# Performance work log

Hardware: AMD Instinct MI355X
Metric: run time of the kernel (lower is better)

## Reference

```python
import jax, jax.numpy as jnp
import numpy as np

B, T, D, H = 2, 2048, 1024, 16
HS = D // H  # head_size = 64


def setup_inputs() -> dict:
    key = jax.random.key(0)
    ks = jax.random.split(key, 8)
    scale = D ** -0.5
    q = jax.random.normal(ks[0], (B, T, D), dtype=jnp.float32)
    k = jax.random.normal(ks[1], (B, T, D), dtype=jnp.float32)
    v = jax.random.normal(ks[2], (B, T, D), dtype=jnp.float32)
    # per-head projection weights (no bias), stacked over heads: [H, D, HS]
    Wq = jax.random.normal(ks[3], (H, D, HS), dtype=jnp.float32) * scale
    Wk = jax.random.normal(ks[4], (H, D, HS), dtype=jnp.float32) * scale
    Wv = jax.random.normal(ks[5], (H, D, HS), dtype=jnp.float32) * scale
    # output projection Linear(H*HS, D) with bias
    Wo = jax.random.normal(ks[6], (D, D), dtype=jnp.float32) * scale
    bo = jnp.zeros((D,), dtype=jnp.float32)
    # causal mask, broadcastable to [B, T, T]; mask==0 -> -inf
    mask = jnp.tril(jnp.ones((T, T), dtype=bool))[None]
    return {"q": q, "k": k, "v": v, "Wq": Wq, "Wk": Wk, "Wv": Wv,
            "Wo": Wo, "bo": bo, "mask": mask}


def reference(q, k, v, Wq, Wk, Wv, Wo, bo, mask):
    # Batched equivalent of the per-head loop: project all heads at once.
    Q = jnp.einsum('btc,hcd->bhtd', q, Wq)  # [B,H,T,HS]
    K = jnp.einsum('btc,hcd->bhtd', k, Wk)
    V = jnp.einsum('btc,hcd->bhtd', v, Wv)
    wei = jnp.einsum('bhtd,bhsd->bhts', Q, K) * (HS ** -0.5)  # [B,H,T,T]
    wei = jnp.where(mask[:, None, :, :], wei, jnp.float32(-jnp.inf))
    attn = jax.nn.softmax(wei, axis=-1)  # dropout is identity in eval
    out = jnp.einsum('bhts,bhsd->bhtd', attn, V)
    out = out.transpose(0, 2, 1, 3).reshape(B, T, D)  # concat heads
    return out @ Wo + bo
```

## Files before the change

kernel.cpp:

```cpp
#include <hip/hip_runtime.h>
#include <hip/hip_bf16.h>
#include <math.h>

#define BB 2
#define TT 2048
#define DM 1024
#define NH 16
#define HS 64
#define MM (BB*TT)

typedef __attribute__((ext_vector_type(8))) short s16x8;
typedef __attribute__((ext_vector_type(4))) float f32x4;

#define MFMA16(a,b,c) __builtin_amdgcn_mfma_f32_16x16x32_bf16((a),(b),(c),0,0,0)

__device__ inline unsigned short f2bf(float f) {
    union { float f; unsigned u; } x; x.f = f;
    unsigned r = x.u + 0x7fff + ((x.u >> 16) & 1);
    return (unsigned short)(r >> 16);
}
__device__ inline unsigned short f2bfr(float f) {
    union { float f; unsigned u; } x; x.f = f;
    return (unsigned short)((x.u + 0x8000u) >> 16);
}

__device__ __forceinline__ void gload16(const void* g, void* l) {
    __builtin_amdgcn_global_load_lds(
        (const __attribute__((address_space(1))) unsigned int*)g,
        (__attribute__((address_space(3))) unsigned int*)l, 16, 0, 0);
}

__global__ __launch_bounds__(256) void cvt_w_kernel(
    const float* __restrict__ W0, const float* __restrict__ W1,
    const float* __restrict__ W2, unsigned short* __restrict__ dst, int wo_mode)
{
    __shared__ __align__(16) short Tt[64 * 72];
    const int t = threadIdx.x;
    const int d0 = blockIdx.x * 64;
    const int h  = blockIdx.y;
    const int z  = blockIdx.z;
    const float* W = (z == 0) ? W0 : (z == 1) ? W1 : W2;
    unsigned short* dz = dst + (size_t)z * DM * DM;

    const int hs4 = (t & 15) * 4;
    const int dl0 = t >> 4;
    #pragma unroll
    for (int it = 0; it < 4; ++it) {
        int dl = it * 16 + dl0;
        const float* src = wo_mode
            ? &W[(size_t)(d0 + dl) * DM + h * 64 + hs4]
            : &W[(size_t)h * DM * HS + (size_t)(d0 + dl) * HS + hs4];
        float4 vv = *(const float4*)src;
        Tt[(hs4 + 0) * 72 + dl] = (short)f2bf(vv.x);
        Tt[(hs4 + 1) * 72 + dl] = (short)f2bf(vv.y);
        Tt[(hs4 + 2) * 72 + dl] = (short)f2bf(vv.z);
        Tt[(hs4 + 3) * 72 + dl] = (short)f2bf(vv.w);
    }
    __syncthreads();
    int hs = t >> 2, doff = (t & 3) * 16;
    s16x8 r0 = *(s16x8*)&Tt[hs * 72 + doff];
    s16x8 r1 = *(s16x8*)&Tt[hs * 72 + doff + 8];
    unsigned short* op = dz + (size_t)(h * 64 + hs) * DM + d0 + doff;
    *(s16x8*)op = r0;
    *(s16x8*)(op + 8) = r1;
}

__global__ __launch_bounds__(512) void proj_gemm_kernel(
    const float* __restrict__ q, const float* __restrict__ k,
    const float* __restrict__ v, const unsigned short* __restrict__ Wt,
    unsigned short* __restrict__ Qb, unsigned short* __restrict__ Kb,
    unsigned short* __restrict__ Vt)
{
    __shared__ __align__(16) unsigned short As[2][128 * 32];
    __shared__ __align__(16) unsigned short Bs[2][128 * 32];

    const int tid = threadIdx.x;
    const int l = tid & 63, w = tid >> 6;
    const int wr = w >> 2, wc = w & 3;
    const int g = l >> 4, r16 = l & 15;

    const int bid = blockIdx.x;
    const int xcd = bid & 7, u = bid >> 3;
    const int z = u >> 5, vv = u & 31;
    const int n0 = (vv >> 2) * 128;
    const int m0 = (xcd * 4 + (vv & 3)) * 128;

    const float* x = (z == 0) ? q : (z == 1) ? k : v;
    const unsigned short* Wz = Wt + (size_t)z * DM * DM;

    const int ar = tid >> 2, aq = tid & 3;
    const float* axp = x + (size_t)(m0 + ar) * DM + aq * 8;
    const int axr = (ar >> 1) & 3;
    const int awof = ar * 32 + ((aq ^ axr) * 8);

    const int brow = tid >> 2, bgl = tid & 3;
    const unsigned short* bS = Wz + (size_t)(n0 + brow) * DM
                             + ((bgl ^ ((brow >> 1) & 3)) * 8);
    const int bDof = tid * 8;

    int aoff[4], boff[2];
    #pragma unroll
    for (int i = 0; i < 4; ++i) {
        int row = wr * 64 + i * 16 + r16;
        aoff[i] = row * 32 + ((g ^ ((row >> 1) & 3)) * 8);
    }
    #pragma unroll
    for (int c = 0; c < 2; ++c) {
        int row = wc * 32 + c * 16 + r16;
        boff[c] = row * 32 + ((g ^ ((row >> 1) & 3)) * 8);
    }

    f32x4 acc[4][2];
    #pragma unroll
    for (int i = 0; i < 4; ++i)
        #pragma unroll
        for (int c = 0; c < 2; ++c)
            #pragma unroll
            for (int j = 0; j < 4; ++j) acc[i][c][j] = 0.0f;

    float4 al0, al1;

    #define PLOADA(k0_) do {                                             \
        const float* ap = axp + (k0_);                                   \
        al0 = *(const float4*)(ap);                                      \
        al1 = *(const float4*)(ap + 4);                                  \
    } while (0)

    #define GLOADB(buf, k0_) gload16(bS + (k0_), &Bs[(buf)][bDof])

    #define PSTORE(buf) do {                                             \
        union { s16x8 v; __hip_bfloat162 h[4]; } c0;                     \
        c0.h[0] = __float22bfloat162_rn(make_float2(al0.x, al0.y));      \
        c0.h[1] = __float22bfloat162_rn(make_float2(al0.z, al0.w));      \
        c0.h[2] = __float22bfloat162_rn(make_float2(al1.x, al1.y));      \
        c0.h[3] = __float22bfloat162_rn(make_float2(al1.z, al1.w));      \
        *(s16x8*)&As[(buf)][awof] = c0.v;                                \
    } while (0)

    #define PCOMPUTE(buf) do {                                           \
        s16x8 af[4], bf[2];                                              \
        _Pragma("unroll")                                                \
        for (int i = 0; i < 4; ++i) af[i] = *(const s16x8*)&As[(buf)][aoff[i]]; \
        _Pragma("unroll")                                                \
        for (int c = 0; c < 2; ++c) bf[c] = *(const s16x8*)&Bs[(buf)][boff[c]]; \
        _Pragma("unroll")                                                \
        for (int i = 0; i < 4; ++i)                                      \
            _Pragma("unroll")                                            \
            for (int c = 0; c < 2; ++c)                                  \
                acc[i][c] = MFMA16(af[i], bf[c], acc[i][c]);             \
    } while (0)

    PLOADA(0);
    GLOADB(0, 0);
    PSTORE(0);
    for (int t = 0; t < 31; ++t) {
        const int cur = t & 1;
        PLOADA((t + 1) * 32);
        GLOADB(cur ^ 1, (t + 1) * 32);
        asm volatile("s_waitcnt vmcnt(3) lgkmcnt(0)" ::: "memory");
        __builtin_amdgcn_sched_barrier(0);
        __builtin_amdgcn_s_barrier();
        PCOMPUTE(cur);
        PSTORE(cur ^ 1);
        __builtin_amdgcn_s_barrier();
    }
    asm volatile("s_waitcnt vmcnt(0) lgkmcnt(0)" ::: "memory");
    __builtin_amdgcn_sched_barrier(0);
    __builtin_amdgcn_s_barrier();
    PCOMPUTE(1);
    #undef PLOADA
    #undef GLOADB
    #undef PSTORE
    #undef PCOMPUTE

    const int h = (n0 >> 6) + (wc >> 1);
    const int hsb = (wc & 1) * 32;
    if (z != 2) {
        unsigned short* dst = (z == 0) ? Qb : Kb;
        const float sc = (z == 0) ? 0.18033688011112042f : 1.0f;
        #pragma unroll
        for (int i = 0; i < 4; ++i)
            #pragma unroll
            for (int j = 0; j < 4; ++j) {
                int row = m0 + wr * 64 + i * 16 + g * 4 + j;
                int bb = row >> 11, tt = row & (TT - 1);
                size_t rb = (((size_t)(bb * NH + h)) * TT + tt) * HS;
                #pragma unroll
                for (int c = 0; c < 2; ++c)
                    dst[rb + hsb + c * 16 + r16] = f2bf(acc[i][c][j] * sc);
            }
    } else {
        #pragma unroll
        for (int i = 0; i < 4; ++i) {
            int row0 = m0 + wr * 64 + i * 16 + g * 4;
            int bb = row0 >> 11, tt0 = row0 & (TT - 1);
            #pragma unroll
            for (int c = 0; c < 2; ++c) {
                int hs = hsb + c * 16 + r16;
                union { unsigned long long u; unsigned short s[4]; } pk;
                #pragma unroll
                for (int j = 0; j < 4; ++j) pk.s[j] = f2bf(acc[i][c][j]);
                *(unsigned long long*)&Vt[(((size_t)(bb * NH + h)) * HS + hs) * TT + tt0] = pk.u;
            }
        }
    }
}

__global__ __launch_bounds__(512) void out_gemm_kernel(
    const unsigned short* __restrict__ Ob, const unsigned short* __restrict__ Wot,
    const float* __restrict__ bo, float* __restrict__ out)
{
    __shared__ __align__(16) unsigned short As2[2][128 * 32];
    __shared__ __align__(16) unsigned short Bs2[2][128 * 32];

    const int tid = threadIdx.x;
    const int l = tid & 63, w = tid >> 6;
    const int wr = w >> 2, wc = w & 3;
    const int g = l >> 4, r16 = l & 15;

    const int bid = blockIdx.x;
    const int xcd = bid & 7, u = bid >> 3;
    const int n0 = (u >> 2) * 128;
    const int m0 = (xcd * 4 + (u & 3)) * 128;

    const int srow = tid >> 2, sgl = tid & 3;
    const int scol = ((sgl ^ ((srow >> 1) & 3)) * 8);
    const unsigned short* aS = Ob + (size_t)(m0 + srow) * DM + scol;
    const unsigned short* bS = Wot + (size_t)(n0 + srow) * DM + scol;
    const int sDof = tid * 8;

    int aoff[4], boff[2];
    #pragma unroll
    for (int i = 0; i < 4; ++i) {
        int row = wr * 64 + i * 16 + r16;
        aoff[i] = row * 32 + ((g ^ ((row >> 1) & 3)) * 8);
    }
    #pragma unroll
    for (int c = 0; c < 2; ++c) {
        int row = wc * 32 + c * 16 + r16;
        boff[c] = row * 32 + ((g ^ ((row >> 1) & 3)) * 8);
    }

    f32x4 acc[4][2];
    #pragma unroll
    for (int i = 0; i < 4; ++i)
        #pragma unroll
        for (int c = 0; c < 2; ++c)
            #pragma unroll
            for (int j = 0; j < 4; ++j) acc[i][c][j] = 0.0f;

    #define OSTAGE(buf, k0_) do {                                        \
        gload16(aS + (k0_), &As2[(buf)][sDof]);                          \
        gload16(bS + (k0_), &Bs2[(buf)][sDof]);                          \
    } while (0)

    #define OCOMPUTE(buf) do {                                           \
        s16x8 af[4], bf[2];                                              \
        _Pragma("unroll")                                                \
        for (int i = 0; i < 4; ++i) af[i] = *(const s16x8*)&As2[(buf)][aoff[i]]; \
        _Pragma("unroll")                                                \
        for (int c = 0; c < 2; ++c) bf[c] = *(const s16x8*)&Bs2[(buf)][boff[c]]; \
        _Pragma("unroll")                                                \
        for (int i = 0; i < 4; ++i)                                      \
            _Pragma("unroll")                                            \
            for (int c = 0; c < 2; ++c)                                  \
                acc[i][c] = MFMA16(af[i], bf[c], acc[i][c]);             \
    } while (0)

    OSTAGE(0, 0);
    for (int t = 0; t < 31; ++t) {
        OSTAGE((t + 1) & 1, (t + 1) * 32);
        asm volatile("s_waitcnt vmcnt(2)" ::: "memory");
        __builtin_amdgcn_sched_barrier(0);
        __builtin_amdgcn_s_barrier();
        OCOMPUTE(t & 1);
        __builtin_amdgcn_s_barrier();
    }
    asm volatile("s_waitcnt vmcnt(0)" ::: "memory");
    __builtin_amdgcn_sched_barrier(0);
    __builtin_amdgcn_s_barrier();
    OCOMPUTE(1);
    #undef OSTAGE
    #undef OCOMPUTE

    #pragma unroll
    for (int i = 0; i < 4; ++i)
        #pragma unroll
        for (int j = 0; j < 4; ++j) {
            int row = m0 + wr * 64 + i * 16 + g * 4 + j;
            #pragma unroll
            for (int c = 0; c < 2; ++c) {
                int col = n0 + wc * 32 + c * 16 + r16;
                out[(size_t)row * DM + col] = acc[i][c][j] + bo[col];
            }
        }
}

template<bool MASKED>
__device__ __forceinline__ void ftile9(
    int kv0, int t0, int r16, int g,
    const unsigned short* __restrict__ Kl,
    const unsigned short* __restrict__ Vl,
    short* __restrict__ Pw0, short* __restrict__ Pw1,
    const s16x8 (&qf)[2],
    float& l_run, f32x4 (&o)[4])
{
    const int rs = r16 & 7;
    const bool half1 = !MASKED || (kv0 + 32 <= t0 + 15);
    float pe[4][4];
    __builtin_amdgcn_s_setprio(1);
    f32x4 s0a[4];
    #pragma unroll
    for (int c = 0; c < 4; ++c) {
        if (!MASKED || (kv0 + c * 16 <= t0 + 15)) {
            f32x4 s0;
            #pragma unroll
            for (int j = 0; j < 4; ++j) s0[j] = 0.0f;
            const int base = (c * 16 + r16) * 64;
            s16x8 kf0 = *(const s16x8*)&Kl[base + ((g ^ rs) * 8)];
            s16x8 kf1 = *(const s16x8*)&Kl[base + (((4 + g) ^ rs) * 8)];
            s0 = MFMA16(kf0, qf[0], s0);
            s0 = MFMA16(kf1, qf[1], s0);
            s0a[c] = s0;
        }
    }
    __builtin_amdgcn_s_setprio(0);
    #pragma unroll
    for (int c = 0; c < 4; ++c) {
        if (!MASKED || (kv0 + c * 16 <= t0 + 15)) {
            #pragma unroll
            for (int j = 0; j < 4; ++j) {
                float e = __builtin_amdgcn_exp2f(s0a[c][j] - 16.0f);
                if (MASKED)
                    e = (kv0 + c * 16 + g * 4 + j <= t0 + r16) ? e : 0.0f;
                pe[c][j] = e;
                l_run += e;
            }
        } else {
            #pragma unroll
            for (int j = 0; j < 4; ++j) pe[c][j] = 0.0f;
        }
    }

    #pragma unroll
    for (int c = 0; c < 2; ++c) {
        union { unsigned long long u; unsigned short s[4]; } pk;
        #pragma unroll
        for (int j = 0; j < 4; ++j) pk.s[j] = f2bfr(pe[c][j]);
        *(unsigned long long*)&Pw0[r16 * 36 + c * 16 + g * 4] = pk.u;
    }
    if (half1) {
        #pragma unroll
        for (int c = 0; c < 2; ++c) {
            union { unsigned long long u; unsigned short s[4]; } pk;
            #pragma unroll
            for (int j = 0; j < 4; ++j) pk.s[j] = f2bfr(pe[2 + c][j]);
            *(unsigned long long*)&Pw1[r16 * 36 + c * 16 + g * 4] = pk.u;
        }
    }
    s16x8 pb0 = *(const s16x8*)&Pw0[r16 * 36 + g * 8];
    __builtin_amdgcn_s_setprio(1);
    #pragma unroll
    for (int c = 0; c < 4; ++c) {
        s16x8 vf = *(const s16x8*)&Vl[(c * 16 + r16) * 64 + ((g ^ rs) * 8)];
        o[c] = MFMA16(vf, pb0, o[c]);
    }
    if (half1) {
        s16x8 pb1 = *(const s16x8*)&Pw1[r16 * 36 + g * 8];
        #pragma unroll
        for (int c = 0; c < 4; ++c) {
            s16x8 vf = *(const s16x8*)&Vl[(c * 16 + r16) * 64 + (((4 + g) ^ rs) * 8)];
            o[c] = MFMA16(vf, pb1, o[c]);
        }
    }
    __builtin_amdgcn_s_setprio(0);
}

__global__ __launch_bounds__(512) void flash9_kernel(
    const unsigned short* __restrict__ Qb,
    const unsigned short* __restrict__ Kb,
    const unsigned short* __restrict__ Vt,
    unsigned short* __restrict__ Ob)
{
    __shared__ __align__(16) unsigned short Kls[2][4096];
    __shared__ __align__(16) unsigned short Vls[2][4096];
    __shared__ __align__(16) short Pl[8][2][576];

    const int tid = threadIdx.x;
    const int l = tid & 63, w = tid >> 6;
    const int r16 = l & 15, g = l >> 4;

    const int bid = blockIdx.x;
    const int bh = bid & 31;
    const int jj = bid >> 5;
    const int qc = (jj < 8) ? (15 - jj) : (jj - 8);
    const int numt = 2 * qc + 2;
    const int b = bh >> 4, h = bh & 15;

    const unsigned short* Qp = Qb + (size_t)bh * TT * HS;
    const unsigned short* Kp = Kb + (size_t)bh * TT * HS;
    const unsigned short* Vp = Vt + (size_t)bh * HS * TT;
    unsigned short* Op = Ob + (size_t)b * TT * DM + h * HS;
    short* Pw0 = &Pl[w][0][0];
    short* Pw1 = &Pl[w][1][0];

    const int t0 = qc * 128 + w * 16;

    const int srow = tid >> 3, c8 = tid & 7;
    const unsigned short* kS = Kp + srow * HS + ((c8 ^ (srow & 7)) * 8);
    const unsigned short* vS = Vp + (size_t)srow * TT + ((c8 ^ (srow & 7)) * 8);
    const int d0 = tid * 8;

    s16x8 qf[2];
    #pragma unroll
    for (int s = 0; s < 2; ++s)
        qf[s] = *(const s16x8*)(Qp + (size_t)(t0 + r16) * HS + s * 32 + g * 8);

    float l_run = 0.0f;
    f32x4 o[4];
    #pragma unroll
    for (int c = 0; c < 4; ++c)
        #pragma unroll
        for (int j = 0; j < 4; ++j) o[c][j] = 0.0f;

    #define STAGE(buf, kv0_) do {                                   \
        gload16(kS + (size_t)(kv0_) * HS, &Kls[(buf)][d0]);         \
        gload16(vS + (kv0_), &Vls[(buf)][d0]);                      \
    } while (0)

    #define FTILE(kv0_, buf_) do {                                  \
        if ((kv0_) + 64 <= t0 + 1)                                  \
            ftile9<false>((kv0_), t0, r16, g, &Kls[(buf_)][0],      \
                          &Vls[(buf_)][0], Pw0, Pw1, qf, l_run, o); \
        else if ((kv0_) <= t0 + 15)                                 \
            ftile9<true>((kv0_), t0, r16, g, &Kls[(buf_)][0],       \
                         &Vls[(buf_)][0], Pw0, Pw1, qf, l_run, o);  \
    } while (0)

    STAGE(0, 0);
    for (int t = 0; t < numt - 1; ++t) {
        STAGE((t + 1) & 1, (t + 1) * 64);
        asm volatile("s_waitcnt vmcnt(2)" ::: "memory");
        __builtin_amdgcn_sched_barrier(0);
        __builtin_amdgcn_s_barrier();
        FTILE(t * 64, t & 1);
        __builtin_amdgcn_s_barrier();
    }
    asm volatile("s_waitcnt vmcnt(0)" ::: "memory");
    __builtin_amdgcn_sched_barrier(0);
    __builtin_amdgcn_s_barrier();
    FTILE((numt - 1) * 64, (numt - 1) & 1);
    #undef STAGE
    #undef FTILE

    float ls = l_run;
    ls += __shfl_xor(ls, 16);
    ls += __shfl_xor(ls, 32);
    const float inv = 1.0f / ls;
    unsigned short* rp = Op + (size_t)(t0 + r16) * DM;
    #pragma unroll
    for (int c = 0; c < 4; ++c) {
        union { unsigned long long u; unsigned short s[4]; } pk;
        #pragma unroll
        for (int j = 0; j < 4; ++j) pk.s[j] = f2bfr(o[c][j] * inv);
        *(unsigned long long*)&rp[c * 16 + g * 4] = pk.u;
    }
}

extern "C" void kernel_launch(void* const* d_in, const int* in_sizes, int n_in,
                              void* d_out, int out_size, void* d_ws, size_t ws_size,
                              hipStream_t stream) {
    const float* q  = (const float*)d_in[0];
    const float* k  = (const float*)d_in[1];
    const float* v  = (const float*)d_in[2];
    const float* Wq = (const float*)d_in[3];
    const float* Wk = (const float*)d_in[4];
    const float* Wv = (const float*)d_in[5];
    const float* Wo = (const float*)d_in[6];
    const float* bo = (const float*)d_in[7];
    float* out = (float*)d_out;

    const size_t QKV_ELEMS = (size_t)BB * NH * TT * HS;
    unsigned short* Qb = (unsigned short*)d_ws;
    unsigned short* Kb = Qb + QKV_ELEMS;
    unsigned short* Vt = Kb + QKV_ELEMS;
    unsigned short* R4 = Vt + QKV_ELEMS;
    unsigned short* Wt = R4;
    unsigned short* Ob = R4;
    unsigned short* Wot = Qb;

    cvt_w_kernel<<<dim3(16, 16, 3), 256, 0, stream>>>(Wq, Wk, Wv, Wt, 0);
    proj_gemm_kernel<<<dim3(768), 512, 0, stream>>>(q, k, v, Wt, Qb, Kb, Vt);
    flash9_kernel<<<dim3(512), 512, 0, stream>>>(Qb, Kb, Vt, Ob);
    cvt_w_kernel<<<dim3(16, 16, 1), 256, 0, stream>>>(Wo, Wo, Wo, Wot, 1);
    out_gemm_kernel<<<dim3(256), 512, 0, stream>>>(Ob, Wot, bo, out);
}
```

Measured before the change: 121.0 us.

## Pre-convert activations to bf16 and use 256x256 tiles in projection GEMM

Adds a separate kernel that converts the fp32 q/k/v activations to bf16 in a workspace, so the projection GEMM can stage both operands with direct global-to-LDS loads. The projection kernel moves to 256x256 output tiles with K-step 64, a double-buffered split-half staging schedule interleaved with four MFMA phases, and s_setprio around the MFMA bursts. This raises data reuse per block and removes the in-loop fp32-to-bf16 conversion, but adds an extra launch plus a full read and write of the activations. It also drops to 192 blocks, which may underfill 256 CUs.

```diff
diff --git a/kernel.cpp b/kernel.cpp
--- a/kernel.cpp
+++ b/kernel.cpp
@@ -65,138 +65,151 @@
     *(s16x8*)(op + 8) = r1;
 }
 
-__global__ __launch_bounds__(512) void proj_gemm_kernel(
+__global__ __launch_bounds__(256) void cvt_x_kernel(
     const float* __restrict__ q, const float* __restrict__ k,
-    const float* __restrict__ v, const unsigned short* __restrict__ Wt,
+    const float* __restrict__ v, unsigned short* __restrict__ xb)
+{
+    const int z = blockIdx.z;
+    const float* x = (z == 0) ? q : (z == 1) ? k : v;
+    unsigned short* d = xb + (size_t)z * MM * DM;
+    const size_t i = ((size_t)blockIdx.x * 256 + threadIdx.x) * 8;
+    float4 a0 = *(const float4*)&x[i];
+    float4 a1 = *(const float4*)&x[i + 4];
+    union { s16x8 v; __hip_bfloat162 h[4]; } cv;
+    cv.h[0] = __float22bfloat162_rn(make_float2(a0.x, a0.y));
+    cv.h[1] = __float22bfloat162_rn(make_float2(a0.z, a0.w));
+    cv.h[2] = __float22bfloat162_rn(make_float2(a1.x, a1.y));
+    cv.h[3] = __float22bfloat162_rn(make_float2(a1.z, a1.w));
+    *(s16x8*)&d[i] = cv.v;
+}
+
+__global__ __launch_bounds__(512) void proj8_kernel(
+    const unsigned short* __restrict__ xb, const unsigned short* __restrict__ Wt,
     unsigned short* __restrict__ Qb, unsigned short* __restrict__ Kb,
     unsigned short* __restrict__ Vt)
 {
-    __shared__ __align__(16) unsigned short As[2][128 * 32];
-    __shared__ __align__(16) unsigned short Bs[2][128 * 32];
+    __shared__ __align__(16) unsigned short As[2][2][128 * 64];
+    __shared__ __align__(16) unsigned short Bs[2][2][128 * 64];
 
     const int tid = threadIdx.x;
     const int l = tid & 63, w = tid >> 6;
     const int wr = w >> 2, wc = w & 3;
     const int g = l >> 4, r16 = l & 15;
+    const int r7 = r16 & 7;
+    const int wch = wc >> 1, wc64 = (wc & 1) * 64;
 
     const int bid = blockIdx.x;
-    const int xcd = bid & 7, u = bid >> 3;
-    const int z = u >> 5, vv = u & 31;
-    const int n0 = (vv >> 2) * 128;
-    const int m0 = (xcd * 4 + (vv & 3)) * 128;
-
-    const float* x = (z == 0) ? q : (z == 1) ? k : v;
+    const int xcd = bid & 7, q2 = bid >> 3;
+    const int z = q2 >> 3, q3 = q2 & 7;
+    const int m0 = (xcd * 2 + (q3 >> 2)) * 256;
+    const int n0 = (q3 & 3) * 256;
+
+    const unsigned short* Az = xb + (size_t)z * MM * DM;
     const unsigned short* Wz = Wt + (size_t)z * DM * DM;
 
-    const int ar = tid >> 2, aq = tid & 3;
-    const float* axp = x + (size_t)(m0 + ar) * DM + aq * 8;
-    const int axr = (ar >> 1) & 3;
-    const int awof = ar * 32 + ((aq ^ axr) * 8);
-
-    const int brow = tid >> 2, bgl = tid & 3;
-    const unsigned short* bS = Wz + (size_t)(n0 + brow) * DM
-                             + ((bgl ^ ((brow >> 1) & 3)) * 8);
-    const int bDof = tid * 8;
-
-    int aoff[4], boff[2];
-    #pragma unroll
-    for (int i = 0; i < 4; ++i) {
-        int row = wr * 64 + i * 16 + r16;
-        aoff[i] = row * 32 + ((g ^ ((row >> 1) & 3)) * 8);
-    }
-    #pragma unroll
-    for (int c = 0; c < 2; ++c) {
-        int row = wc * 32 + c * 16 + r16;
-        boff[c] = row * 32 + ((g ^ ((row >> 1) & 3)) * 8);
-    }
-
-    f32x4 acc[4][2];
-    #pragma unroll
-    for (int i = 0; i < 4; ++i)
-        #pragma unroll
-        for (int c = 0; c < 2; ++c)
+    const unsigned short* aG[2]; const unsigned short* bG[2]; int dO[2];
+    #pragma unroll
+    for (int p = 0; p < 2; ++p) {
+        int qid = p * 512 + tid;
+        int srow = qid >> 3, scp = qid & 7;
+        int scol = (scp ^ (srow & 7)) * 8;
+        aG[p] = Az + (size_t)(m0 + srow) * DM + scol;
+        bG[p] = Wz + (size_t)(n0 + srow) * DM + scol;
+        dO[p] = qid * 8;
+    }
+
+    f32x4 acc[8][4];
+    #pragma unroll
+    for (int i = 0; i < 8; ++i)
+        #pragma unroll
+        for (int c = 0; c < 4; ++c)
             #pragma unroll
             for (int j = 0; j < 4; ++j) acc[i][c][j] = 0.0f;
 
-    float4 al0, al1;
-
-    #define PLOADA(k0_) do {                                             \
-        const float* ap = axp + (k0_);                                   \
-        al0 = *(const float4*)(ap);                                      \
-        al1 = *(const float4*)(ap + 4);                                  \
-    } while (0)
-
-    #define GLOADB(buf, k0_) gload16(bS + (k0_), &Bs[(buf)][bDof])
-
-    #define PSTORE(buf) do {                                             \
-        union { s16x8 v; __hip_bfloat162 h[4]; } c0;                     \
-        c0.h[0] = __float22bfloat162_rn(make_float2(al0.x, al0.y));      \
-        c0.h[1] = __float22bfloat162_rn(make_float2(al0.z, al0.w));      \
-        c0.h[2] = __float22bfloat162_rn(make_float2(al1.x, al1.y));      \
-        c0.h[3] = __float22bfloat162_rn(make_float2(al1.z, al1.w));      \
-        *(s16x8*)&As[(buf)][awof] = c0.v;                                \
-    } while (0)
-
-    #define PCOMPUTE(buf) do {                                           \
-        s16x8 af[4], bf[2];                                              \
-        _Pragma("unroll")                                                \
-        for (int i = 0; i < 4; ++i) af[i] = *(const s16x8*)&As[(buf)][aoff[i]]; \
-        _Pragma("unroll")                                                \
-        for (int c = 0; c < 2; ++c) bf[c] = *(const s16x8*)&Bs[(buf)][boff[c]]; \
-        _Pragma("unroll")                                                \
-        for (int i = 0; i < 4; ++i)                                      \
-            _Pragma("unroll")                                            \
-            for (int c = 0; c < 2; ++c)                                  \
-                acc[i][c] = MFMA16(af[i], bf[c], acc[i][c]);             \
-    } while (0)
-
-    PLOADA(0);
-    GLOADB(0, 0);
-    PSTORE(0);
-    for (int t = 0; t < 31; ++t) {
-        const int cur = t & 1;
-        PLOADA((t + 1) * 32);
-        GLOADB(cur ^ 1, (t + 1) * 32);
-        asm volatile("s_waitcnt vmcnt(3) lgkmcnt(0)" ::: "memory");
+    #define STAGE_A(buf, hh, kel) do {                                   \
+        _Pragma("unroll")                                                 \
+        for (int p = 0; p < 2; ++p)                                       \
+            gload16(aG[p] + (size_t)(hh) * 128 * DM + (kel),              \
+                    &As[(buf)][(hh)][dO[p]]);                             \
+    } while (0)
+    #define STAGE_B(buf, hh, kel) do {                                   \
+        _Pragma("unroll")                                                 \
+        for (int p = 0; p < 2; ++p)                                       \
+            gload16(bG[p] + (size_t)(hh) * 128 * DM + (kel),              \
+                    &Bs[(buf)][(hh)][dO[p]]);                             \
+    } while (0)
+
+    #define PHASE(bufv, MG, NG) do {                                      \
+        s16x8 af[4][2], bf[2][2];                                          \
+        const unsigned short* Ab = &As[(bufv)][wr][0];                     \
+        const unsigned short* Bb = &Bs[(bufv)][wch][0];                    \
+        _Pragma("unroll")                                                  \
+        for (int i2 = 0; i2 < 4; ++i2) {                                   \
+            int r = ((MG) * 4 + i2) * 16 + r16;                            \
+            af[i2][0] = *(const s16x8*)&Ab[r * 64 + (((0 + g) ^ r7) * 8)]; \
+            af[i2][1] = *(const s16x8*)&Ab[r * 64 + (((4 + g) ^ r7) * 8)]; \
+        }                                                                  \
+        _Pragma("unroll")                                                  \
+        for (int c2 = 0; c2 < 2; ++c2) {                                   \
+            int r = wc64 + ((NG) * 2 + c2) * 16 + r16;                     \
+            bf[c2][0] = *(const s16x8*)&Bb[r * 64 + (((0 + g) ^ r7) * 8)]; \
+            bf[c2][1] = *(const s16x8*)&Bb[r * 64 + (((4 + g) ^ r7) * 8)]; \
+        }                                                                  \
+        __builtin_amdgcn_s_setprio(1);                                     \
+        _Pragma("unroll")                                                  \
+        for (int i2 = 0; i2 < 4; ++i2)                                     \
+            _Pragma("unroll")                                              \
+            for (int c2 = 0; c2 < 2; ++c2) {                               \
+                acc[(MG)*4+i2][(NG)*2+c2] = MFMA16(af[i2][0], bf[c2][0],   \
+                    acc[(MG)*4+i2][(NG)*2+c2]);                            \
+                acc[(MG)*4+i2][(NG)*2+c2] = MFMA16(af[i2][1], bf[c2][1],   \
+                    acc[(MG)*4+i2][(NG)*2+c2]);                            \
+            }                                                              \
+        __builtin_amdgcn_s_setprio(0);                                     \
+    } while (0)
+
+    STAGE_A(0, 0, 0); STAGE_A(0, 1, 0);
+    STAGE_B(0, 0, 0); STAGE_B(0, 1, 0);
+
+    for (int t = 0; t < 16; ++t) {
+        const int buf = t & 1, nb = buf ^ 1;
+        asm volatile("s_waitcnt vmcnt(0)" ::: "memory");
         __builtin_amdgcn_sched_barrier(0);
         __builtin_amdgcn_s_barrier();
-        PCOMPUTE(cur);
-        PSTORE(cur ^ 1);
-        __builtin_amdgcn_s_barrier();
-    }
-    asm volatile("s_waitcnt vmcnt(0) lgkmcnt(0)" ::: "memory");
-    __builtin_amdgcn_sched_barrier(0);
-    __builtin_amdgcn_s_barrier();
-    PCOMPUTE(1);
-    #undef PLOADA
-    #undef GLOADB
-    #undef PSTORE
-    #undef PCOMPUTE
-
-    const int h = (n0 >> 6) + (wc >> 1);
-    const int hsb = (wc & 1) * 32;
+        if (t < 15) { STAGE_A(nb, 0, (t + 1) * 64); STAGE_A(nb, 1, (t + 1) * 64); }
+        PHASE(buf, 0, 0);
+        if (t < 15) { STAGE_B(nb, 0, (t + 1) * 64); STAGE_B(nb, 1, (t + 1) * 64); }
+        PHASE(buf, 0, 1);
+        PHASE(buf, 1, 0);
+        PHASE(buf, 1, 1);
+    }
+    #undef STAGE_A
+    #undef STAGE_B
+    #undef PHASE
+
+    const int h = (n0 >> 6) + wc;
     if (z != 2) {
         unsigned short* dst = (z == 0) ? Qb : Kb;
         const float sc = (z == 0) ? 0.18033688011112042f : 1.0f;
         #pragma unroll
-        for (int i = 0; i < 4; ++i)
+        for (int i = 0; i < 8; ++i)
             #pragma unroll
             for (int j = 0; j < 4; ++j) {
-                int row = m0 + wr * 64 + i * 16 + g * 4 + j;
+                int row = m0 + wr * 128 + i * 16 + g * 4 + j;
                 int bb = row >> 11, tt = row & (TT - 1);
                 size_t rb = (((size_t)(bb * NH + h)) * TT + tt) * HS;
                 #pragma unroll
-                for (int c = 0; c < 2; ++c)
-                    dst[rb + hsb + c * 16 + r16] = f2bf(acc[i][c][j] * sc);
+                for (int c = 0; c < 4; ++c)
+                    dst[rb + c * 16 + r16] = f2bf(acc[i][c][j] * sc);
             }
     } else {
         #pragma unroll
-        for (int i = 0; i < 4; ++i) {
-            int row0 = m0 + wr * 64 + i * 16 + g * 4;
+        for (int i = 0; i < 8; ++i) {
+            int row0 = m0 + wr * 128 + i * 16 + g * 4;
             int bb = row0 >> 11, tt0 = row0 & (TT - 1);
             #pragma unroll
-            for (int c = 0; c < 2; ++c) {
-                int hs = hsb + c * 16 + r16;
+            for (int c = 0; c < 4; ++c) {
+                int hs = c * 16 + r16;
                 union { unsigned long long u; unsigned short s[4]; } pk;
                 #pragma unroll
                 for (int j = 0; j < 4; ++j) pk.s[j] = f2bf(acc[i][c][j]);
@@ -488,9 +501,11 @@
     unsigned short* Wt = R4;
     unsigned short* Ob = R4;
     unsigned short* Wot = Qb;
+    unsigned short* xb = R4 + QKV_ELEMS;
 
     cvt_w_kernel<<<dim3(16, 16, 3), 256, 0, stream>>>(Wq, Wk, Wv, Wt, 0);
-    proj_gemm_kernel<<<dim3(768), 512, 0, stream>>>(q, k, v, Wt, Qb, Kb, Vt);
+    cvt_x_kernel<<<dim3(2048, 1, 3), 256, 0, stream>>>(q, k, v, xb);
+    proj8_kernel<<<dim3(192), 512, 0, stream>>>(xb, Wt, Qb, Kb, Vt);
     flash9_kernel<<<dim3(512), 512, 0, stream>>>(Qb, Kb, Vt, Ob);
     cvt_w_kernel<<<dim3(16, 16, 1), 256, 0, stream>>>(Wo, Wo, Wo, Wot, 1);
     out_gemm_kernel<<<dim3(256), 512, 0, stream>>>(Ob, Wot, bo, out);
```

Result: slower. 136.8 us (+13.0%).

## Double K-tile depth in projection GEMM to 64 and raise MFMA priority

Applied to the files above, without the earlier changes.

The projection GEMM's K step per iteration grows from 32 to 64, so each thread loads four float4s of activations and two async B chunks per stage. The LDS swizzle changes to a 3-bit XOR over eight 16-byte chunks. Halving the iteration count cuts barriers and loop overhead per MFMA. s_setprio is also raised around the MFMA block. The cost is twice the LDS footprint (64KB), which may reduce occupancy, plus more live registers.

```diff
diff --git a/kernel.cpp b/kernel.cpp
--- a/kernel.cpp
+++ b/kernel.cpp
@@ -71,13 +71,14 @@
     unsigned short* __restrict__ Qb, unsigned short* __restrict__ Kb,
     unsigned short* __restrict__ Vt)
 {
-    __shared__ __align__(16) unsigned short As[2][128 * 32];
-    __shared__ __align__(16) unsigned short Bs[2][128 * 32];
+    __shared__ __align__(16) unsigned short As[2][128 * 64];
+    __shared__ __align__(16) unsigned short Bs[2][128 * 64];
 
     const int tid = threadIdx.x;
     const int l = tid & 63, w = tid >> 6;
     const int wr = w >> 2, wc = w & 3;
     const int g = l >> 4, r16 = l & 15;
+    const int r7 = r16 & 7;
 
     const int bid = blockIdx.x;
     const int xcd = bid & 7, u = bid >> 3;
@@ -89,25 +90,31 @@
     const unsigned short* Wz = Wt + (size_t)z * DM * DM;
 
     const int ar = tid >> 2, aq = tid & 3;
-    const float* axp = x + (size_t)(m0 + ar) * DM + aq * 8;
-    const int axr = (ar >> 1) & 3;
-    const int awof = ar * 32 + ((aq ^ axr) * 8);
-
-    const int brow = tid >> 2, bgl = tid & 3;
-    const unsigned short* bS = Wz + (size_t)(n0 + brow) * DM
-                             + ((bgl ^ ((brow >> 1) & 3)) * 8);
-    const int bDof = tid * 8;
-
-    int aoff[4], boff[2];
+    const float* axp = x + (size_t)(m0 + ar) * DM + aq * 16;
+    const int awof0 = ar * 64 + (((aq * 2)     ^ (ar & 7)) * 8);
+    const int awof1 = ar * 64 + (((aq * 2 + 1) ^ (ar & 7)) * 8);
+
+    const unsigned short* bS[2]; int bDof[2];
+    #pragma unroll
+    for (int p = 0; p < 2; ++p) {
+        int qid = p * 512 + tid;
+        int brow = qid >> 3, bcp = qid & 7;
+        bS[p] = Wz + (size_t)(n0 + brow) * DM + ((bcp ^ (brow & 7)) * 8);
+        bDof[p] = qid * 8;
+    }
+
+    int aoff[4][2], boff[2][2];
     #pragma unroll
     for (int i = 0; i < 4; ++i) {
         int row = wr * 64 + i * 16 + r16;
-        aoff[i] = row * 32 + ((g ^ ((row >> 1) & 3)) * 8);
+        aoff[i][0] = row * 64 + (((0 + g) ^ r7) * 8);
+        aoff[i][1] = row * 64 + (((4 + g) ^ r7) * 8);
     }
     #pragma unroll
     for (int c = 0; c < 2; ++c) {
         int row = wc * 32 + c * 16 + r16;
-        boff[c] = row * 32 + ((g ^ ((row >> 1) & 3)) * 8);
+        boff[c][0] = row * 64 + (((0 + g) ^ r7) * 8);
+        boff[c][1] = row * 64 + (((4 + g) ^ r7) * 8);
     }
 
     f32x4 acc[4][2];
@@ -118,46 +125,66 @@
             #pragma unroll
             for (int j = 0; j < 4; ++j) acc[i][c][j] = 0.0f;
 
-    float4 al0, al1;
+    float4 al0, al1, al2, al3;
 
     #define PLOADA(k0_) do {                                             \
         const float* ap = axp + (k0_);                                   \
         al0 = *(const float4*)(ap);                                      \
         al1 = *(const float4*)(ap + 4);                                  \
-    } while (0)
-
-    #define GLOADB(buf, k0_) gload16(bS + (k0_), &Bs[(buf)][bDof])
+        al2 = *(const float4*)(ap + 8);                                  \
+        al3 = *(const float4*)(ap + 12);                                 \
+    } while (0)
+
+    #define GLOADB(buf, k0_) do {                                        \
+        gload16(bS[0] + (k0_), &Bs[(buf)][bDof[0]]);                     \
+        gload16(bS[1] + (k0_), &Bs[(buf)][bDof[1]]);                     \
+    } while (0)
 
     #define PSTORE(buf) do {                                             \
-        union { s16x8 v; __hip_bfloat162 h[4]; } c0;                     \
-        c0.h[0] = __float22bfloat162_rn(make_float2(al0.x, al0.y));      \
-        c0.h[1] = __float22bfloat162_rn(make_float2(al0.z, al0.w));      \
-        c0.h[2] = __float22bfloat162_rn(make_float2(al1.x, al1.y));      \
-        c0.h[3] = __float22bfloat162_rn(make_float2(al1.z, al1.w));      \
-        *(s16x8*)&As[(buf)][awof] = c0.v;                                \
+        union { s16x8 v; __hip_bfloat162 h2[4]; } c0, c1;                \
+        c0.h2[0] = __float22bfloat162_rn(make_float2(al0.x, al0.y));     \
+        c0.h2[1] = __float22bfloat162_rn(make_float2(al0.z, al0.w));     \
+        c0.h2[2] = __float22bfloat162_rn(make_float2(al1.x, al1.y));     \
+        c0.h2[3] = __float22bfloat162_rn(make_float2(al1.z, al1.w));     \
+        c1.h2[0] = __float22bfloat162_rn(make_float2(al2.x, al2.y));     \
+        c1.h2[1] = __float22bfloat162_rn(make_float2(al2.z, al2.w));     \
+        c1.h2[2] = __float22bfloat162_rn(make_float2(al3.x, al3.y));     \
+        c1.h2[3] = __float22bfloat162_rn(make_float2(al3.z, al3.w));     \
+        *(s16x8*)&As[(buf)][awof0] = c0.v;                               \
+        *(s16x8*)&As[(buf)][awof1] = c1.v;                               \
     } while (0)
 
     #define PCOMPUTE(buf) do {                                           \
-        s16x8 af[4], bf[2];                                              \
+        s16x8 af[4][2], bf[2][2];                                        \
         _Pragma("unroll")                                                \
-        for (int i = 0; i < 4; ++i) af[i] = *(const s16x8*)&As[(buf)][aoff[i]]; \
+        for (int i = 0; i < 4; ++i) {                                    \
+            af[i][0] = *(const s16x8*)&As[(buf)][aoff[i][0]];            \
+            af[i][1] = *(const s16x8*)&As[(buf)][aoff[i][1]];            \
+        }                                                                \
         _Pragma("unroll")                                                \
-        for (int c = 0; c < 2; ++c) bf[c] = *(const s16x8*)&Bs[(buf)][boff[c]]; \
+        for (int c = 0; c < 2; ++c) {                                    \
+            bf[c][0] = *(const s16x8*)&Bs[(buf)][boff[c][0]];            \
+            bf[c][1] = *(const s16x8*)&Bs[(buf)][boff[c][1]];            \
+        }                                                                \
+        __builtin_amdgcn_s_setprio(1);                                   \
         _Pragma("unroll")                                                \
         for (int i = 0; i < 4; ++i)                                      \
             _Pragma("unroll")                                            \
-            for (int c = 0; c < 2; ++c)                                  \
-                acc[i][c] = MFMA16(af[i], bf[c], acc[i][c]);             \
+            for (int c = 0; c < 2; ++c) {                                \
+                acc[i][c] = MFMA16(af[i][0], bf[c][0], acc[i][c]);       \
+                acc[i][c] = MFMA16(af[i][1], bf[c][1], acc[i][c]);       \
+            }                                                            \
+        __builtin_amdgcn_s_setprio(0);                                   \
     } while (0)
 
     PLOADA(0);
     GLOADB(0, 0);
     PSTORE(0);
-    for (int t = 0; t < 31; ++t) {
+    for (int t = 0; t < 15; ++t) {
         const int cur = t & 1;
-        PLOADA((t + 1) * 32);
-        GLOADB(cur ^ 1, (t + 1) * 32);
-        asm volatile("s_waitcnt vmcnt(3) lgkmcnt(0)" ::: "memory");
+        PLOADA((t + 1) * 64);
+        GLOADB(cur ^ 1, (t + 1) * 64);
+        asm volatile("s_waitcnt vmcnt(6) lgkmcnt(0)" ::: "memory");
         __builtin_amdgcn_sched_barrier(0);
         __builtin_amdgcn_s_barrier();
         PCOMPUTE(cur);
```

After: 131.1 us. 1.08x slower.
